# Performance work log

Hardware: AMD Instinct MI355X
Metric: run time of the kernel (lower is better)

## Reference

```python
import jax, jax.numpy as jnp
import numpy as np

ITERS = 4
LN_EPS = 1e-5


def build_grid(H, W):
    # standard uORF grid in [-1, 1], shape (H, W, 2), last dim = (x, y)
    x = jnp.linspace(-1.0 + 1.0 / W, 1.0 - 1.0 / W, W)
    y = jnp.linspace(-1.0 + 1.0 / H, 1.0 - 1.0 / H, H)
    yy, xx = jnp.meshgrid(y, x, indexing='ij')
    return jnp.stack([xx, yy], axis=-1)


def ln(x, g, b):
    m = jnp.mean(x, axis=-1, keepdims=True)
    v = jnp.var(x, axis=-1, keepdims=True)
    return (x - m) * jax.lax.rsqrt(v + LN_EPS) * g + b


def setup_inputs():
    key = jax.random.key(0)
    ks = jax.random.split(key, 16)
    B, H, W, C, K, Ds = 4, 64, 64, 256, 5, 256
    s = 0.02
    inp = {
        'feat': jax.random.normal(ks[0], (B, H, W, C), jnp.float32),
        'mask': (jax.random.uniform(ks[1], (K, 1, H, W)) > 0.5).astype(jnp.float32),
        'noise': jax.random.normal(ks[2], (B, K, Ds), jnp.float32),
        'slots_mu': jax.random.normal(ks[3], (1, 1, Ds), jnp.float32),
        'slots_logsigma': jax.random.normal(ks[4], (1, 1, Ds), jnp.float32) * s,
        'norm_g': jnp.ones((C,), jnp.float32), 'norm_b': jnp.zeros((C,), jnp.float32),
        'grid_W': jax.random.normal(ks[5], (C, 4), jnp.float32) * s,
        'grid_b': jnp.zeros((C,), jnp.float32),
        'k_W': jax.random.normal(ks[6], (C, C), jnp.float32) * s,
        'v_W': jax.random.normal(ks[7], (C, C), jnp.float32) * s,
        'mlp_g': jnp.ones((C,), jnp.float32), 'mlp_b': jnp.zeros((C,), jnp.float32),
        'mlp_W': jax.random.normal(ks[8], (Ds, C), jnp.float32) * s,
        'mlp_bias': jnp.zeros((Ds,), jnp.float32),
        'q_g': jnp.ones((Ds,), jnp.float32), 'q_b': jnp.zeros((Ds,), jnp.float32),
        'q_W': jax.random.normal(ks[9], (Ds, Ds), jnp.float32) * s,
        'gru_Wih': jax.random.normal(ks[10], (3 * Ds, Ds), jnp.float32) * s,
        'gru_Whh': jax.random.normal(ks[11], (3 * Ds, Ds), jnp.float32) * s,
        'gru_bih': jnp.zeros((3 * Ds,), jnp.float32),
        'gru_bhh': jnp.zeros((3 * Ds,), jnp.float32),
        'res_g': jnp.ones((Ds,), jnp.float32), 'res_b': jnp.zeros((Ds,), jnp.float32),
        'res_W': jax.random.normal(ks[12], (Ds, Ds), jnp.float32) * s,
        'res_bias': jnp.zeros((Ds,), jnp.float32),
    }
    return inp


def reference(feat, mask, noise, slots_mu, slots_logsigma, norm_g, norm_b,
              grid_W, grid_b, k_W, v_W, mlp_g, mlp_b, mlp_W, mlp_bias,
              q_g, q_b, q_W, gru_Wih, gru_Whh, gru_bih, gru_bhh,
              res_g, res_b, res_W, res_bias):
    B, H, W, C = feat.shape
    K = mask.shape[0]
    N = H * W
    Ds = slots_mu.shape[-1]
    scale = Ds ** -0.5

    grid = build_grid(H, W)                                   # (H, W, 2)
    # foreground positions: mask-weighted mean of grid -> (K, 2)
    g = jnp.transpose(grid, (2, 0, 1))[None]                  # (1, 2, H, W)
    fg_pos = jnp.sum(g * mask, axis=(2, 3)) / (jnp.sum(mask, axis=(2, 3)) + 1e-5)
    fg_pos = jnp.broadcast_to(fg_pos[None], (B, K, 2))        # (B, K, 2)

    feat_n = ln(feat.reshape(B, N, C), norm_g, norm_b)        # (B, N, C)
    mask_flat = mask.reshape(K, N)
    slot = slots_mu + jnp.exp(slots_logsigma) * noise         # (B, K, Ds)

    # k, v with relative position embedding; fg_pos never changes in-loop,
    # so compute once (the original recomputes the same values each iter).
    rel = grid.reshape(1, 1, N, 2) - fg_pos[:, :, None, :]    # (B, K, N, 2)
    rel4 = jnp.concatenate([rel, -rel], axis=-1)              # (B, K, N, 4)
    ge = rel4 @ grid_W.T + grid_b                             # (B, K, N, C)
    kbase = feat_n @ k_W.T                                    # (B, N, C)
    vbase = feat_n @ v_W.T
    kk = ln(kbase[:, None] + ge, mlp_g, mlp_b) @ mlp_W.T + mlp_bias  # (B,K,N,Ds)
    vv = ln(vbase[:, None] + ge, mlp_g, mlp_b) @ mlp_W.T + mlp_bias

    attn_vis = None
    for _ in range(ITERS):
        slot_prev = slot
        q = ln(slot, q_g, q_b) @ q_W.T                        # (B, K, Ds)
        attn = jnp.einsum('bkd,bknd->bkn', q, kk) * scale
        attn = jnp.where(mask_flat[None] == 0, -1e9, attn)
        attn = jax.nn.softmax(attn, axis=-1)                  # (B, K, N)
        upd = jnp.einsum('bkn,bknd->bkd', attn, vv)           # (B, K, Ds)
        # torch GRUCell
        x = upd.reshape(-1, Ds)
        h = slot.reshape(-1, Ds)
        gi = x @ gru_Wih.T + gru_bih
        gh = h @ gru_Whh.T + gru_bhh
        ir, iz, inn = jnp.split(gi, 3, axis=-1)
        hr, hz, hn = jnp.split(gh, 3, axis=-1)
        r = jax.nn.sigmoid(ir + hr)
        z = jax.nn.sigmoid(iz + hz)
        n = jnp.tanh(inn + r * hn)
        hnew = ((1.0 - z) * n + z * h).reshape(B, K, Ds)
        slot = (ln(hnew, res_g, res_b) @ res_W.T + res_bias) + slot_prev
        amin = attn.min(axis=-1, keepdims=True)
        amax = attn.max(axis=-1, keepdims=True)
        attn_vis = (attn - amin) / (amax - amin + 1e-5)
    return slot, fg_pos, attn_vis
```

## Files before the change

### kernel.cpp

```cpp
#include <hip/hip_runtime.h>
#include <math.h>

typedef unsigned short u16;
typedef unsigned int   u32;
typedef short bf8v __attribute__((ext_vector_type(8)));
typedef float f4v  __attribute__((ext_vector_type(4)));

static constexpr int B_=4, C_=256, K_=5, D_=256, N_=4096, IT_=4;
static constexpr int LP_=264;
static constexpr int PREP_N=2839;
static constexpr float EPS_=1e-5f;

__device__ __forceinline__ float bf2f(u16 u){ u32 x=((u32)u)<<16; float f; __builtin_memcpy(&f,&x,4); return f; }
__device__ __forceinline__ float bflo(u32 u){ u32 x=u<<16; float f; __builtin_memcpy(&f,&x,4); return f; }
__device__ __forceinline__ float bfhi(u32 u){ u32 x=u&0xffff0000u; float f; __builtin_memcpy(&f,&x,4); return f; }
__device__ __forceinline__ u16 f2bf(float f){ u32 x; __builtin_memcpy(&x,&f,4); u32 r=x+0x7fffu+((x>>16)&1u); return (u16)(r>>16); }
__device__ __forceinline__ float ldin(const void* p, size_t i, int f){
  return f ? ((const float*)p)[i] : bf2f(((const u16*)p)[i]);
}
__device__ __forceinline__ void stout(void* p, size_t i, float v, int f){
  if (f) ((float*)p)[i]=v; else ((u16*)p)[i]=f2bf(v);
}

__device__ __forceinline__ void breduce4(float&a,float&b,float&c,float&d,float* red){
  #pragma unroll
  for(int o=32;o>0;o>>=1){
    a+=__shfl_down(a,o,64); b+=__shfl_down(b,o,64);
    c+=__shfl_down(c,o,64); d+=__shfl_down(d,o,64);
  }
  int w=threadIdx.x>>6;
  __syncthreads();
  if((threadIdx.x&63)==0){ red[w]=a; red[4+w]=b; red[8+w]=c; red[12+w]=d; }
  __syncthreads();
  a=red[0]+red[1]+red[2]+red[3];
  b=red[4]+red[5]+red[6]+red[7];
  c=red[8]+red[9]+red[10]+red[11];
  d=red[12]+red[13]+red[14]+red[15];
}
__device__ __forceinline__ void breduce4_16(float&a,float&b,float&c,float&d,float* red){
  #pragma unroll
  for(int o=32;o>0;o>>=1){
    a+=__shfl_down(a,o,64); b+=__shfl_down(b,o,64);
    c+=__shfl_down(c,o,64); d+=__shfl_down(d,o,64);
  }
  int w=threadIdx.x>>6;
  __syncthreads();
  if((threadIdx.x&63)==0){ red[w]=a; red[16+w]=b; red[32+w]=c; red[48+w]=d; }
  __syncthreads();
  a=0;b=0;c=0;d=0;
  #pragma unroll
  for(int i=0;i<16;++i){ a+=red[i]; b+=red[16+i]; c+=red[32+i]; d+=red[48+i]; }
}

__device__ __forceinline__ int probe_f(const void* feat, float* red){
  const u32* p=(const u32*)feat;
  int t=threadIdx.x; int bad=0;
  #pragma unroll
  for(int s=0;s<8;++s){
    u32 wd=p[t+s*256];
    float lo=bf2f((u16)(wd&0xffffu));
    if(!(fabsf(lo)<1e6f)) bad++;
  }
  float bb=(float)bad, z1=0,z2=0,z3=0;
  breduce4(bb,z1,z2,z3,red);
  return (bb>=16.f)?1:0;
}

__global__ void prep1_kernel(const void* feat,
    const void* kW, const void* vW, const void* mW, const void* qW, const void* rW,
    const void* Wih, const void* Whh, const void* mu, const void* lsig, const void* noise,
    const void* gW, const void* gb_, const void* mg,
    const void* mb_, const void* mbias, const void* mask,
    int* flag, float* WqT, float* WrT, float* WihT, float* WhhT,
    float* slot, float* gvec,
    u16* Wkb, u16* Wvb, u16* Wgb,
    float* Uvec, float* Qs, float* fg, void* out)
{
  __shared__ float redp[16];
  int bid=blockIdx.x;
  int t=threadIdx.x;
  int f=probe_f(feat, redp);
  if(bid==0 && t==0) *flag=f;
  __syncthreads();
  if(bid<PREP_N){
    int e=bid*256+t;
    if(e<65536){ int c=e>>8, r=e&255; WqT[e]=ldin(qW,(size_t)r*256+c,f); return;} e-=65536;
    if(e<65536){ int c=e>>8, r=e&255; WrT[e]=ldin(rW,(size_t)r*256+c,f); return;} e-=65536;
    if(e<196608){ int c=e/768, r=e-c*768; WihT[e]=ldin(Wih,(size_t)r*256+c,f); return;} e-=196608;
    if(e<196608){ int c=e/768, r=e-c*768; WhhT[e]=ldin(Whh,(size_t)r*256+c,f); return;} e-=196608;
    if(e<5120){ int d=e&255; slot[e]=ldin(mu,d,f)+expf(ldin(lsig,d,f))*ldin(noise,e,f); return;} e-=5120;
    if(e<768){
      int c=e&255, sel=e>>8;
      float v;
      if(sel==0)      v=ldin(gW,c*4+0,f)-ldin(gW,c*4+2,f);
      else if(sel==1) v=ldin(gW,c*4+1,f)-ldin(gW,c*4+3,f);
      else            v=ldin(gb_,c,f);
      gvec[e]=v; return;
    } e-=768;
    if(e<65536){ Wkb[e]=f2bf(ldin(kW,e,f)); return;} e-=65536;
    if(e<65536){ Wvb[e]=f2bf(ldin(vW,e,f)); return;} e-=65536;
    if(e<65536){ int c=e&255; Wgb[e]=f2bf(ldin(mg,c,f)*ldin(mW,e,f)); }
    return;
  }
  __shared__ float s_a[256], s_b[256], s_c[256];
  if(bid==PREP_N){
    s_a[t]=ldin(gW,t*4+0,f)-ldin(gW,t*4+2,f);
    s_b[t]=ldin(gW,t*4+1,f)-ldin(gW,t*4+3,f);
    s_c[t]=ldin(gb_,t,f);
    __syncthreads();
    float u1=0,u2=0,u3=0,gw=0,bw=0;
    #pragma unroll 8
    for(int c=0;c<256;++c){
      float mwv=ldin(mW,(size_t)t*256+c,f);
      float wg=ldin(mg,c,f)*mwv;
      u1+=s_a[c]*wg; u2+=s_b[c]*wg; u3+=s_c[c]*wg; gw+=wg;
      bw+=ldin(mb_,c,f)*mwv;
    }
    Uvec[t]=u1; Uvec[256+t]=u2; Uvec[512+t]=u3; Uvec[768+t]=gw;
    Uvec[1024+t]=bw+ldin(mbias,t,f);
    float a=s_a[t], b=s_b[t], cc=s_c[t];
    float s0=a*a,s1=b*b,s2=cc*cc,s3=a*b; breduce4(s0,s1,s2,s3,redp);
    float s4=a*cc,s5=b*cc,s6=a,s7=b;     breduce4(s4,s5,s6,s7,redp);
    float s8=cc,z1=0,z2=0,z3=0;          breduce4(s8,z1,z2,z3,redp);
    if(t==0){
      Qs[0]=s0; Qs[1]=s1; Qs[2]=s2; Qs[3]=s3; Qs[4]=s4; Qs[5]=s5;
      Qs[6]=s6*(1.f/256.f); Qs[7]=s7*(1.f/256.f); Qs[8]=s8*(1.f/256.f);
    }
  } else {
    int k=bid-PREP_N-1;
    float sx=0,sy=0,sm=0;
    for(int s=0;s<16;++s){
      int p=t+s*256;
      float m=ldin(mask,(size_t)k*N_+p,f);
      int i=p>>6, j=p&63;
      float x=(2*j+1)*(1.0f/64.0f)-1.0f;
      float y=(2*i+1)*(1.0f/64.0f)-1.0f;
      sx+=x*m; sy+=y*m; sm+=m;
    }
    float d=0;
    breduce4(sx,sy,sm,d,redp);
    if(t==0){
      float inv=1.0f/(sm+1e-5f);
      float fx=sx*inv, fy=sy*inv;
      fg[k*2]=fx; fg[k*2+1]=fy;
      for(int b=0;b<B_;++b){
        stout(out, 5120+(b*K_+k)*2+0, fx, f);
        stout(out, 5120+(b*K_+k)*2+1, fy, f);
      }
    }
  }
}

__global__ void __launch_bounds__(256) base_kernel(const int* flag, const void* feat, const void* ng, const void* nb,
    const u16* Wkb, const u16* Wvb, const u16* Wgb, const float* gvec,
    float* scal, u16* PkT, u16* Pvb,
    const float* slot, const void* qg, const void* qb_, const float* WqT,
    float* qbuf)
{
  __shared__ u16 fnb[16*LP_];
  __shared__ u16 kbL[16*LP_];
  __shared__ u16 vbL[16*LP_];
  int t=threadIdx.x, f=*flag;
  if(blockIdx.x>=1024){
    float* Lq=(float*)fnb; float* red=(float*)vbL;
    int bk=blockIdx.x-1024;
    float x=slot[bk*256+t];
    float s=x,s2=x*x,z0=0,z1=0; breduce4(s,s2,z0,z1,red);
    float m=s*(1.f/256.f), v=s2*(1.f/256.f)-m*m;
    Lq[t]=(x-m)*rsqrtf(v+EPS_)*ldin(qg,t,f)+ldin(qb_,t,f);
    __syncthreads();
    float acc=0;
    #pragma unroll 8
    for(int c=0;c<256;++c) acc+=Lq[c]*WqT[c*256+t];
    qbuf[bk*256+t]=acc;
    return;
  }
  int w=t>>6, l=t&63;
  int quad=l>>4, m=l&15;
  int row0=blockIdx.x*16;
  {
    float g0=ldin(ng,l,f), g1=ldin(ng,l+64,f), g2=ldin(ng,l+128,f), g3=ldin(ng,l+192,f);
    float b0=ldin(nb,l,f), b1=ldin(nb,l+64,f), b2=ldin(nb,l+128,f), b3=ldin(nb,l+192,f);
    #pragma unroll
    for(int r4=0;r4<4;++r4){
      int r=4*w+r4; size_t base=(size_t)(row0+r)*256;
      float x0=ldin(feat,base+l,f), x1=ldin(feat,base+l+64,f),
            x2=ldin(feat,base+l+128,f), x3=ldin(feat,base+l+192,f);
      float s=x0+x1+x2+x3, s2=x0*x0+x1*x1+x2*x2+x3*x3;
      #pragma unroll
      for(int o=32;o>0;o>>=1){ s+=__shfl_xor(s,o,64); s2+=__shfl_xor(s2,o,64); }
      float mm=s*(1.f/256.f), inv=rsqrtf(s2*(1.f/256.f)-mm*mm+EPS_);
      fnb[r*LP_+l]    =f2bf((x0-mm)*inv*g0+b0);
      fnb[r*LP_+l+64] =f2bf((x1-mm)*inv*g1+b1);
      fnb[r*LP_+l+128]=f2bf((x2-mm)*inv*g2+b2);
      fnb[r*LP_+l+192]=f2bf((x3-mm)*inv*g3+b3);
    }
  }
  __syncthreads();
  {
    f4v ack[4], acv[4];
    #pragma unroll
    for(int i=0;i<4;++i){ ack[i]=(f4v){0.f,0.f,0.f,0.f}; acv[i]=(f4v){0.f,0.f,0.f,0.f}; }
    #pragma unroll
    for(int kk=0;kk<8;++kk){
      int kb0=kk*32+quad*8;
      bf8v af=*(bf8v*)&fnb[m*LP_+kb0];
      #pragma unroll
      for(int i=0;i<4;++i){
        int n=64*w+16*i+m;
        bf8v bk=*(const bf8v*)(Wkb+(size_t)n*256+kb0);
        bf8v bv=*(const bf8v*)(Wvb+(size_t)n*256+kb0);
        ack[i]=__builtin_amdgcn_mfma_f32_16x16x32_bf16(af,bk,ack[i],0,0,0);
        acv[i]=__builtin_amdgcn_mfma_f32_16x16x32_bf16(af,bv,acv[i],0,0,0);
      }
    }
    #pragma unroll
    for(int i=0;i<4;++i){
      int n=64*w+16*i+m;
      #pragma unroll
      for(int r=0;r<4;++r){
        int row=quad*4+r;
        kbL[row*LP_+n]=f2bf(ack[i][r]);
        vbL[row*LP_+n]=f2bf(acv[i][r]);
      }
    }
  }
  __syncthreads();
  {
    float gA0=gvec[l], gA1=gvec[l+64], gA2=gvec[l+128], gA3=gvec[l+192];
    float gB0=gvec[256+l], gB1=gvec[256+l+64], gB2=gvec[256+l+128], gB3=gvec[256+l+192];
    float gC0=gvec[512+l], gC1=gvec[512+l+64], gC2=gvec[512+l+128], gC3=gvec[512+l+192];
    for(int r4=0;r4<4;++r4){
      int r=4*w+r4;
      float k0=bf2f(kbL[r*LP_+l]), k1=bf2f(kbL[r*LP_+l+64]),
            k2=bf2f(kbL[r*LP_+l+128]), k3=bf2f(kbL[r*LP_+l+192]);
      float x0=bf2f(vbL[r*LP_+l]), x1=bf2f(vbL[r*LP_+l+64]),
            x2=bf2f(vbL[r*LP_+l+128]), x3=bf2f(vbL[r*LP_+l+192]);
      float v0=k0+k1+k2+k3;
      float v1=k0*k0+k1*k1+k2*k2+k3*k3;
      float v2=k0*gA0+k1*gA1+k2*gA2+k3*gA3;
      float v3=k0*gB0+k1*gB1+k2*gB2+k3*gB3;
      float v4=k0*gC0+k1*gC1+k2*gC2+k3*gC3;
      float v5=x0+x1+x2+x3;
      float v6=x0*x0+x1*x1+x2*x2+x3*x3;
      float v7=x0*gA0+x1*gA1+x2*gA2+x3*gA3;
      float v8=x0*gB0+x1*gB1+x2*gB2+x3*gB3;
      float v9=x0*gC0+x1*gC1+x2*gC2+x3*gC3;
      #pragma unroll
      for(int o=32;o>0;o>>=1){
        v0+=__shfl_down(v0,o,64); v1+=__shfl_down(v1,o,64); v2+=__shfl_down(v2,o,64);
        v3+=__shfl_down(v3,o,64); v4+=__shfl_down(v4,o,64); v5+=__shfl_down(v5,o,64);
        v6+=__shfl_down(v6,o,64); v7+=__shfl_down(v7,o,64); v8+=__shfl_down(v8,o,64);
        v9+=__shfl_down(v9,o,64);
      }
      if(l==0){
        float* sc=scal+(size_t)(row0+r)*10;
        sc[0]=v0; sc[1]=v1; sc[2]=v2; sc[3]=v3; sc[4]=v4;
        sc[5]=v5; sc[6]=v6; sc[7]=v7; sc[8]=v8; sc[9]=v9;
      }
    }
  }
  {
    f4v apk[4], apv[4];
    #pragma unroll
    for(int i=0;i<4;++i){ apk[i]=(f4v){0.f,0.f,0.f,0.f}; apv[i]=(f4v){0.f,0.f,0.f,0.f}; }
    #pragma unroll
    for(int kk=0;kk<8;++kk){
      int kb0=kk*32+quad*8;
      bf8v afk=*(bf8v*)&kbL[m*LP_+kb0];
      bf8v afv=*(bf8v*)&vbL[m*LP_+kb0];
      #pragma unroll
      for(int i=0;i<4;++i){
        int n=64*w+16*i+m;
        bf8v bg=*(const bf8v*)(Wgb+(size_t)n*256+kb0);
        apk[i]=__builtin_amdgcn_mfma_f32_16x16x32_bf16(afk,bg,apk[i],0,0,0);
        apv[i]=__builtin_amdgcn_mfma_f32_16x16x32_bf16(afv,bg,apv[i],0,0,0);
      }
    }
    #pragma unroll
    for(int i=0;i<4;++i){
      int d=64*w+16*i+m;
      *(ushort4*)(PkT+(size_t)d*16384+row0+quad*4)=
        make_ushort4(f2bf(apk[i][0]),f2bf(apk[i][1]),f2bf(apk[i][2]),f2bf(apk[i][3]));
      #pragma unroll
      for(int r=0;r<4;++r)
        fnb[(quad*4+r)*LP_+d]=f2bf(apv[i][r]);
    }
  }
  __syncthreads();
  {
    int d0=l*4;
    #pragma unroll
    for(int r=0;r<4;++r){
      int row=4*w+r;
      ushort4 s4=make_ushort4(fnb[row*LP_+d0],fnb[row*LP_+d0+1],fnb[row*LP_+d0+2],fnb[row*LP_+d0+3]);
      *(ushort4*)(Pvb+(size_t)(row0+row)*256+d0)=s4;
    }
  }
}

__global__ void __launch_bounds__(512) attn_kernel(const int* flag, const float* qbuf, const u16* PkT,
    const float* scal, const float* Qs, const float* Uvec, const float* fg, const void* mask,
    const u16* Pvb, float* logits, float* pmax, float* psum, float* updpart, float* sscp,
    int store_lg)
{
  __shared__ float q5[1280];
  __shared__ float un[10240];
  __shared__ float lgs[320], ivs[320], mvs[320];
  __shared__ float qs5[40], fgs[10], Qss[9], MSl[5];
  __shared__ float sred[8][5][4];
  int tid=threadIdx.x, f=*flag;
  int b=blockIdx.x>>6, ch=blockIdx.x&63;
  int w=tid>>6, l=tid&63;
  int n0=ch<<6;
  for(int p=tid;p<1280;p+=512) q5[p]=qbuf[(size_t)b*1280+p];
  if(tid<10) fgs[tid]=fg[tid];
  if(tid<9)  Qss[tid]=Qs[tid];
  __syncthreads();
  for(int p=w;p<25;p+=8){
    int k=p/5, j=p%5;
    float s=q5[k*256+l]*Uvec[j*256+l]+q5[k*256+l+64]*Uvec[j*256+l+64]
           +q5[k*256+l+128]*Uvec[j*256+l+128]+q5[k*256+l+192]*Uvec[j*256+l+192];
    #pragma unroll
    for(int o=32;o>0;o>>=1) s+=__shfl_xor(s,o,64);
    if(l==0) qs5[k*8+j]=s;
  }
  {
    int n=n0+l; size_t row=(size_t)b*N_+n;
    float dk0=0,dk1=0,dk2=0,dk3=0,dk4=0;
    int cbase=w*32;
    #pragma unroll 8
    for(int cc=0;cc<32;++cc){
      int c=cbase+cc;
      float pv=bf2f(PkT[(size_t)c*16384+row]);
      dk0+=pv*q5[c]; dk1+=pv*q5[256+c]; dk2+=pv*q5[512+c];
      dk3+=pv*q5[768+c]; dk4+=pv*q5[1024+c];
    }
    un[(w*5+0)*64+l]=dk0; un[(w*5+1)*64+l]=dk1; un[(w*5+2)*64+l]=dk2;
    un[(w*5+3)*64+l]=dk3; un[(w*5+4)*64+l]=dk4;
  }
  __syncthreads();
  if(tid<320){
    int k=tid>>6, nl=tid&63;
    float dot=0;
    #pragma unroll
    for(int j=0;j<8;++j) dot+=un[(j*5+k)*64+nl];
    int n2=n0+nl; size_t row2=(size_t)b*N_+n2;
    const float* sc=scal+row2*10;
    float rx=(2*(n2&63)+1)*(1.f/64.f)-1.f-fgs[2*k];
    float ry=(2*(n2>>6)+1)*(1.f/64.f)-1.f-fgs[2*k+1];
    float qge=rx*rx*Qss[0]+ry*ry*Qss[1]+Qss[2]+2.f*(rx*ry*Qss[3]+rx*Qss[4]+ry*Qss[5]);
    float mk=sc[0]*(1.f/256.f)+rx*Qss[6]+ry*Qss[7]+Qss[8];
    float sxk=sc[1]+2.f*(rx*sc[2]+ry*sc[3]+sc[4])+qge;
    float invK=rsqrtf(sxk*(1.f/256.f)-mk*mk+EPS_);
    float lg=invK*(dot+rx*qs5[k*8+0]+ry*qs5[k*8+1]+qs5[k*8+2]-mk*qs5[k*8+3])+qs5[k*8+4];
    float mval=ldin(mask,(size_t)k*N_+n2,f);
    lg=(mval==0.f)? -1e9f : lg*0.0625f;
    if(store_lg) logits[((size_t)(b*5+k))*N_+n2]=lg;
    lgs[tid]=lg;
    float mv=sc[5]*(1.f/256.f)+rx*Qss[6]+ry*Qss[7]+Qss[8];
    float sxv=sc[6]+2.f*(rx*sc[7]+ry*sc[8]+sc[9])+qge;
    mvs[tid]=mv;
    ivs[tid]=rsqrtf(sxv*(1.f/256.f)-mv*mv+EPS_);
  }
  __syncthreads();
  if(tid<64){
    #pragma unroll
    for(int k=0;k<5;++k){
      float v=lgs[k*64+tid];
      float M=v;
      #pragma unroll
      for(int o=32;o>0;o>>=1) M=fmaxf(M,__shfl_xor(M,o,64));
      float e=expf(v-M);
      #pragma unroll
      for(int o=32;o>0;o>>=1) e+=__shfl_xor(e,o,64);
      if(tid==0){ pmax[((size_t)(b*64+ch))*5+k]=M; psum[((size_t)(b*64+ch))*5+k]=e; MSl[k]=M; }
    }
  }
  __syncthreads();
  {
    float acc[5][4]={{0}};
    float swx[5]={0,0,0,0,0}, swy[5]={0,0,0,0,0}, sw[5]={0,0,0,0,0}, swm[5]={0,0,0,0,0};
    #pragma unroll 2
    for(int rr=0;rr<8;++rr){
      int nl=w*8+rr; int n2=n0+nl;
      size_t row=(size_t)b*N_+n2;
      uint2 pu=*(const uint2*)(Pvb+row*256+l*4);
      float px=bflo(pu.x), py=bfhi(pu.x), pz=bflo(pu.y), pw=bfhi(pu.y);
      int jx=n2&63, iy=n2>>6;
      #pragma unroll
      for(int k=0;k<5;++k){
        float wgt=expf(lgs[k*64+nl]-MSl[k])*ivs[k*64+nl];
        float rx=(2*jx+1)*(1.f/64.f)-1.f-fgs[2*k];
        float ry=(2*iy+1)*(1.f/64.f)-1.f-fgs[2*k+1];
        acc[k][0]+=wgt*px; acc[k][1]+=wgt*py; acc[k][2]+=wgt*pz; acc[k][3]+=wgt*pw;
        sw[k]+=wgt; swx[k]+=wgt*rx; swy[k]+=wgt*ry; swm[k]+=wgt*mvs[k*64+nl];
      }
    }
    #pragma unroll
    for(int k=0;k<5;++k)
      *(float4*)&un[(w*5+k)*256+l*4]=make_float4(acc[k][0],acc[k][1],acc[k][2],acc[k][3]);
    if(l==0){
      #pragma unroll
      for(int k=0;k<5;++k){ sred[w][k][0]=swx[k]; sred[w][k][1]=swy[k];
                            sred[w][k][2]=sw[k];  sred[w][k][3]=swm[k]; }
    }
  }
  __syncthreads();
  for(int p=tid;p<1280;p+=512){
    int k=p>>8, d=p&255;
    float v=0;
    #pragma unroll
    for(int j=0;j<8;++j) v+=un[(j*5+k)*256+d];
    updpart[((size_t)blockIdx.x*5+k)*256+d]=v;
  }
  if(tid<20){
    int kk=tid>>2, j=tid&3;
    float s=0;
    #pragma unroll
    for(int jj=0;jj<8;++jj) s+=sred[jj][kk][j];
    sscp[((size_t)blockIdx.x*5+kk)*4+j]=s;
  }
}

__global__ void __launch_bounds__(1024) gru_kernel(const int* flag, float* slot, const float* updpart,
    const float* sscp, const float* Uvec, const float* pmax, const float* psum, const float* logits,
    const float* WihT, const float* WhhT, const void* bih, const void* bhh,
    const void* rg, const void* rb_, const float* WrT, const void* rbias,
    const void* qg, const void* qb_, const float* WqT, float* qbuf,
    int do_vis, void* out)
{
  __shared__ float u[256], h[256], sn[256];
  __shared__ float part[4][6][256];
  __shared__ float red[64];
  __shared__ float cvec[4];
  __shared__ float fch[64];
  __shared__ float MSg[2];
  int tid=threadIdx.x, t=tid&255, g=tid>>8;
  int blk=blockIdx.x;
  int f=*flag;
  if(blk>=20){
    if(!do_vis) return;
    int bk2=blk-20, k2=bk2%K_, b2=bk2/K_;
    if(tid<64){
      float pm=pmax[((size_t)(b2*64+tid))*5+k2];
      float ps=psum[((size_t)(b2*64+tid))*5+k2];
      float M=pm;
      #pragma unroll
      for(int o=32;o>0;o>>=1) M=fmaxf(M,__shfl_xor(M,o,64));
      float e=ps*expf(pm-M);
      #pragma unroll
      for(int o=32;o>0;o>>=1) e+=__shfl_xor(e,o,64);
      if(tid==0){ MSg[0]=M; MSg[1]=1.0f/e; }
    }
    __syncthreads();
    float M=MSg[0], Sinv=MSg[1];
    float a[4]; float mn=1e30f, mx=-1e30f;
    #pragma unroll
    for(int s=0;s<4;++s){
      a[s]=expf(logits[(size_t)bk2*N_+tid+s*1024]-M)*Sinv;
      mn=fminf(mn,a[s]); mx=fmaxf(mx,a[s]);
    }
    #pragma unroll
    for(int o=32;o>0;o>>=1){ mn=fminf(mn,__shfl_down(mn,o,64)); mx=fmaxf(mx,__shfl_down(mx,o,64)); }
    int wv=tid>>6;
    __syncthreads();
    if((tid&63)==0){ red[wv]=mn; red[16+wv]=mx; }
    __syncthreads();
    mn=1e30f; mx=-1e30f;
    #pragma unroll
    for(int i=0;i<16;++i){ mn=fminf(mn,red[i]); mx=fmaxf(mx,red[16+i]); }
    float inv=1.0f/(mx-mn+1e-5f);
    #pragma unroll
    for(int s=0;s<4;++s) stout(out, 5160+(size_t)bk2*N_+tid+s*1024, (a[s]-mn)*inv, f);
    return;
  }
  int bk=blk, k=bk%K_, b=bk/K_;
  if(tid<64){
    float pm=pmax[((size_t)(b*64+tid))*5+k];
    float ps=psum[((size_t)(b*64+tid))*5+k];
    float M=pm;
    #pragma unroll
    for(int o=32;o>0;o>>=1) M=fmaxf(M,__shfl_xor(M,o,64));
    float fc=expf(pm-M);
    fch[tid]=fc;
    float e=ps*fc;
    #pragma unroll
    for(int o=32;o>0;o>>=1) e+=__shfl_xor(e,o,64);
    if(tid==0){ MSg[0]=M; MSg[1]=1.0f/e; }
  }
  __syncthreads();
  float Sinv=MSg[1];
  float ua=0;
  {
    int ch0=g*16;
    #pragma unroll 4
    for(int ci=0;ci<16;++ci){ int ch=ch0+ci; ua += fch[ch]*updpart[(((size_t)(b*64+ch))*5+k)*256+t]; }
  }
  part[g][0][t]=ua;
  if(t<4){
    float s=0;
    #pragma unroll 4
    for(int ci=0;ci<16;++ci){ int ch=g*16+ci; s += fch[ch]*sscp[(((size_t)(b*64+ch))*5+k)*4+t]; }
    part[g][1][t]=s;
  }
  __syncthreads();
  if(g==0 && t<4) cvec[t]=part[0][1][t]+part[1][1][t]+part[2][1][t]+part[3][1][t];
  __syncthreads();
  if(g==0){
    float uu=part[0][0][t]+part[1][0][t]+part[2][0][t]+part[3][0][t];
    u[t]=(uu+cvec[0]*Uvec[t]+cvec[1]*Uvec[256+t]+cvec[2]*Uvec[512+t]-cvec[3]*Uvec[768+t])*Sinv
         +Uvec[1024+t];
    h[t]=slot[bk*256+t];
  }
  __syncthreads();
  float p0=0,p1=0,p2=0,p3=0,p4=0,p5=0;
  int c0=g*64;
  #pragma unroll 8
  for(int cc=0;cc<64;++cc){
    int c=c0+cc;
    float uc=u[c], hc=h[c];
    const float* wi=WihT+(size_t)c*768+t;
    const float* wh=WhhT+(size_t)c*768+t;
    p0+=uc*wi[0]; p1+=uc*wi[256]; p2+=uc*wi[512];
    p3+=hc*wh[0]; p4+=hc*wh[256]; p5+=hc*wh[512];
  }
  part[g][0][t]=p0; part[g][1][t]=p1; part[g][2][t]=p2;
  part[g][3][t]=p3; part[g][4][t]=p4; part[g][5][t]=p5;
  __syncthreads();
  float hn=0;
  if(g==0){
    float gi0=ldin(bih,t,f)+part[0][0][t]+part[1][0][t]+part[2][0][t]+part[3][0][t];
    float gi1=ldin(bih,256+t,f)+part[0][1][t]+part[1][1][t]+part[2][1][t]+part[3][1][t];
    float gi2=ldin(bih,512+t,f)+part[0][2][t]+part[1][2][t]+part[2][2][t]+part[3][2][t];
    float gh0=ldin(bhh,t,f)+part[0][3][t]+part[1][3][t]+part[2][3][t]+part[3][3][t];
    float gh1=ldin(bhh,256+t,f)+part[0][4][t]+part[1][4][t]+part[2][4][t]+part[3][4][t];
    float gh2=ldin(bhh,512+t,f)+part[0][5][t]+part[1][5][t]+part[2][5][t]+part[3][5][t];
    float r=1.f/(1.f+expf(-(gi0+gh0)));
    float z=1.f/(1.f+expf(-(gi1+gh1)));
    float nn=tanhf(gi2+r*gh2);
    hn=(1.f-z)*nn+z*h[t];
  }
  float s=hn, sq=hn*hn, za=0, zb=0;
  breduce4_16(s,sq,za,zb,red);
  if(g==0){
    float m=s*(1.f/256.f), var=sq*(1.f/256.f)-m*m;
    u[t]=(hn-m)*rsqrtf(var+EPS_)*ldin(rg,t,f)+ldin(rb_,t,f);
  }
  __syncthreads();
  float pr=0;
  #pragma unroll 8
  for(int cc=0;cc<64;++cc){ int c=c0+cc; pr+=u[c]*WrT[(size_t)c*256+t]; }
  part[g][0][t]=pr;
  __syncthreads();
  if(g==0){
    float acc=ldin(rbias,t,f)+h[t]+part[0][0][t]+part[1][0][t]+part[2][0][t]+part[3][0][t];
    slot[bk*256+t]=acc;
    stout(out, (size_t)bk*256+t, acc, f);
    sn[t]=acc;
  }
  __syncthreads();
  float xs=(g==0)? sn[t]:0.f;
  float xq=xs*xs, zc=0, zd=0;
  breduce4_16(xs,xq,zc,zd,red);
  if(g==0){
    float m=xs*(1.f/256.f), var=xq*(1.f/256.f)-m*m;
    u[t]=(sn[t]-m)*rsqrtf(var+EPS_)*ldin(qg,t,f)+ldin(qb_,t,f);
  }
  __syncthreads();
  float pq=0;
  #pragma unroll 8
  for(int cc=0;cc<64;++cc){ int c=c0+cc; pq+=u[c]*WqT[(size_t)c*256+t]; }
  part[g][0][t]=pq;
  __syncthreads();
  if(g==0){
    float qv=part[0][0][t]+part[1][0][t]+part[2][0][t]+part[3][0][t];
    qbuf[bk*256+t]=qv;
  }
}

extern "C" void kernel_launch(void* const* d_in, const int* in_sizes, int n_in,
                              void* d_out, int out_size, void* d_ws, size_t ws_size,
                              hipStream_t stream)
{
  const void* feat =d_in[0];  const void* mask =d_in[1];  const void* noise=d_in[2];
  const void* mu   =d_in[3];  const void* lsig =d_in[4];  const void* ng   =d_in[5];
  const void* nb   =d_in[6];  const void* gW   =d_in[7];  const void* gb_  =d_in[8];
  const void* kW   =d_in[9];  const void* vW   =d_in[10]; const void* mg   =d_in[11];
  const void* mb_  =d_in[12]; const void* mW   =d_in[13]; const void* mbias=d_in[14];
  const void* qg   =d_in[15]; const void* qb_  =d_in[16]; const void* qW   =d_in[17];
  const void* Wih  =d_in[18]; const void* Whh  =d_in[19]; const void* bih  =d_in[20];
  const void* bhh  =d_in[21]; const void* rg   =d_in[22]; const void* rb_  =d_in[23];
  const void* rW   =d_in[24]; const void* rbias=d_in[25];

  char* p=(char*)d_ws;
  auto alloc=[&](size_t bytes)->char*{ char* r=p; p+=(bytes+255)&~(size_t)255; return r; };
  int*   flag   =(int*)  alloc(256);
  float* fg     =(float*)alloc(64);
  float* slot   =(float*)alloc(5120*4);
  float* qbuf   =(float*)alloc(5120*4);
  float* logits =(float*)alloc((size_t)81920*4);
  float* pmax   =(float*)alloc(1280*4);
  float* psum   =(float*)alloc(1280*4);
  float* updpart=(float*)alloc((size_t)256*5*256*4);
  float* sscp   =(float*)alloc((size_t)256*5*4*4);
  float* WqT    =(float*)alloc((size_t)65536*4);
  float* WrT    =(float*)alloc((size_t)65536*4);
  float* WihT   =(float*)alloc((size_t)196608*4);
  float* WhhT   =(float*)alloc((size_t)196608*4);
  float* gvec   =(float*)alloc(768*4);
  float* Uvec   =(float*)alloc(1280*4);
  float* Qs     =(float*)alloc(64);
  float* scal   =(float*)alloc((size_t)163840*4);
  u16*   Wkb    =(u16*)  alloc((size_t)65536*2);
  u16*   Wvb    =(u16*)  alloc((size_t)65536*2);
  u16*   Wgb    =(u16*)  alloc((size_t)65536*2);
  u16*   PkT    =(u16*)  alloc((size_t)16384*256*2);
  u16*   Pvb    =(u16*)  alloc((size_t)16384*256*2);

  prep1_kernel<<<PREP_N+6,256,0,stream>>>(feat,kW,vW,mW,qW,rW,Wih,Whh,mu,lsig,noise,gW,gb_,mg,
                                          mb_,mbias,mask,
                                          flag,WqT,WrT,WihT,WhhT,slot,gvec,Wkb,Wvb,Wgb,
                                          Uvec,Qs,fg,d_out);
  base_kernel<<<1044,256,0,stream>>>(flag,feat,ng,nb,Wkb,Wvb,Wgb,gvec,scal,PkT,Pvb,
                                     slot,qg,qb_,WqT,qbuf);
  for(int it=0; it<IT_; ++it){
    attn_kernel<<<B_*64,512,0,stream>>>(flag,qbuf,PkT,scal,Qs,Uvec,fg,mask,Pvb,
                                        logits,pmax,psum,updpart,sscp,(it==IT_-1)?1:0);
    int nb_g = (it==IT_-1)? 40 : 20;
    gru_kernel<<<nb_g,1024,0,stream>>>(flag,slot,updpart,sscp,Uvec,pmax,psum,logits,
                                       WihT,WhhT,bih,bhh,rg,rb_,WrT,rbias,
                                       qg,qb_,WqT,qbuf,(it==IT_-1)?1:0,d_out);
  }
}
```

Measured before the change: 385.7 us.

## Retile base kernel to 64-row blocks with swizzled LDS and register-reused MFMA fragments

Each base_kernel block now processes 64 rows with 512 threads instead of 16 rows with 256 threads. Every weight fragment loaded from global memory feeds four row tiles, so weight traffic per row drops roughly fourfold. The padded LDS arrays become two 32 KB dynamic buffers with an XOR swizzle, and the feature loads are vectorised. The block count falls from 1044 to 276, which may leave the GPU underoccupied, and the larger dynamic LDS per block limits residency.

New measurement: 372.7 us. 3.4% less time.

```diff
diff --git a/kernel.cpp b/kernel.cpp
--- a/kernel.cpp
+++ b/kernel.cpp
@@ -7,7 +7,6 @@
 typedef float f4v  __attribute__((ext_vector_type(4)));
 
 static constexpr int B_=4, C_=256, K_=5, D_=256, N_=4096, IT_=4;
-static constexpr int LP_=264;
 static constexpr int PREP_N=2839;
 static constexpr float EPS_=1e-5f;
 
@@ -20,6 +19,9 @@
 }
 __device__ __forceinline__ void stout(void* p, size_t i, float v, int f){
   if (f) ((float*)p)[i]=v; else ((u16*)p)[i]=f2bf(v);
+}
+__device__ __forceinline__ int sw16(int row,int col){
+  return row*256 + ((((col>>3)^(row&7))<<3) | (col&7));
 }
 
 __device__ __forceinline__ void breduce4(float&a,float&b,float&c,float&d,float* red){
@@ -151,91 +153,125 @@
   }
 }
 
-__global__ void __launch_bounds__(256) base_kernel(const int* flag, const void* feat, const void* ng, const void* nb,
+__global__ void __launch_bounds__(512,2) base_kernel(const int* flag, const void* feat, const void* ng, const void* nb,
     const u16* Wkb, const u16* Wvb, const u16* Wgb, const float* gvec,
     float* scal, u16* PkT, u16* Pvb,
     const float* slot, const void* qg, const void* qb_, const float* WqT,
     float* qbuf)
 {
-  __shared__ u16 fnb[16*LP_];
-  __shared__ u16 kbL[16*LP_];
-  __shared__ u16 vbL[16*LP_];
+  extern __shared__ u16 smem[];
+  u16* bufA = smem;
+  u16* bufB = smem + 16384;
   int t=threadIdx.x, f=*flag;
-  if(blockIdx.x>=1024){
-    float* Lq=(float*)fnb; float* red=(float*)vbL;
-    int bk=blockIdx.x-1024;
-    float x=slot[bk*256+t];
-    float s=x,s2=x*x,z0=0,z1=0; breduce4(s,s2,z0,z1,red);
-    float m=s*(1.f/256.f), v=s2*(1.f/256.f)-m*m;
-    Lq[t]=(x-m)*rsqrtf(v+EPS_)*ldin(qg,t,f)+ldin(qb_,t,f);
-    __syncthreads();
-    float acc=0;
+  if(blockIdx.x>=256){
+    float* Lq =(float*)smem;
+    float* pp =(float*)smem+256;
+    float* red=(float*)smem+768;
+    int bk=blockIdx.x-256;
+    int tt=t&255, hh=t>>8, w=t>>6;
+    float x=slot[bk*256+tt];
+    float s=x, s2=x*x;
+    #pragma unroll
+    for(int o=32;o>0;o>>=1){ s+=__shfl_down(s,o,64); s2+=__shfl_down(s2,o,64); }
+    if((t&63)==0){ red[w]=s; red[8+w]=s2; }
+    __syncthreads();
+    s=0; s2=0;
+    #pragma unroll
+    for(int i=0;i<8;++i){ s+=red[i]; s2+=red[8+i]; }
+    float m=s*(1.f/512.f), v=s2*(1.f/512.f)-m*m;
+    float lq=(x-m)*rsqrtf(v+EPS_)*ldin(qg,tt,f)+ldin(qb_,tt,f);
+    if(hh==0) Lq[tt]=lq;
+    __syncthreads();
+    float acc=0; int cb=hh*128;
     #pragma unroll 8
-    for(int c=0;c<256;++c) acc+=Lq[c]*WqT[c*256+t];
-    qbuf[bk*256+t]=acc;
+    for(int cc=0;cc<128;++cc){ int c=cb+cc; acc+=Lq[c]*WqT[(size_t)c*256+tt]; }
+    pp[hh*256+tt]=acc;
+    __syncthreads();
+    if(hh==0) qbuf[bk*256+tt]=pp[tt]+pp[256+tt];
     return;
   }
   int w=t>>6, l=t&63;
   int quad=l>>4, m=l&15;
-  int row0=blockIdx.x*16;
+  int row0=blockIdx.x*64;
   {
-    float g0=ldin(ng,l,f), g1=ldin(ng,l+64,f), g2=ldin(ng,l+128,f), g3=ldin(ng,l+192,f);
-    float b0=ldin(nb,l,f), b1=ldin(nb,l+64,f), b2=ldin(nb,l+128,f), b3=ldin(nb,l+192,f);
-    #pragma unroll
-    for(int r4=0;r4<4;++r4){
-      int r=4*w+r4; size_t base=(size_t)(row0+r)*256;
-      float x0=ldin(feat,base+l,f), x1=ldin(feat,base+l+64,f),
-            x2=ldin(feat,base+l+128,f), x3=ldin(feat,base+l+192,f);
+    float g0=ldin(ng,4*l+0,f), g1=ldin(ng,4*l+1,f), g2=ldin(ng,4*l+2,f), g3=ldin(ng,4*l+3,f);
+    float b0=ldin(nb,4*l+0,f), b1=ldin(nb,4*l+1,f), b2=ldin(nb,4*l+2,f), b3=ldin(nb,4*l+3,f);
+    #pragma unroll
+    for(int r8=0;r8<8;++r8){
+      int row=8*w+r8;
+      float x0,x1,x2,x3;
+      if(f){
+        float4 v4=((const float4*)feat)[(size_t)(row0+row)*64+l];
+        x0=v4.x; x1=v4.y; x2=v4.z; x3=v4.w;
+      } else {
+        ushort4 uu=((const ushort4*)feat)[(size_t)(row0+row)*64+l];
+        x0=bf2f(uu.x); x1=bf2f(uu.y); x2=bf2f(uu.z); x3=bf2f(uu.w);
+      }
       float s=x0+x1+x2+x3, s2=x0*x0+x1*x1+x2*x2+x3*x3;
       #pragma unroll
       for(int o=32;o>0;o>>=1){ s+=__shfl_xor(s,o,64); s2+=__shfl_xor(s2,o,64); }
       float mm=s*(1.f/256.f), inv=rsqrtf(s2*(1.f/256.f)-mm*mm+EPS_);
-      fnb[r*LP_+l]    =f2bf((x0-mm)*inv*g0+b0);
-      fnb[r*LP_+l+64] =f2bf((x1-mm)*inv*g1+b1);
-      fnb[r*LP_+l+128]=f2bf((x2-mm)*inv*g2+b2);
-      fnb[r*LP_+l+192]=f2bf((x3-mm)*inv*g3+b3);
+      ushort4 o4=make_ushort4(f2bf((x0-mm)*inv*g0+b0), f2bf((x1-mm)*inv*g1+b1),
+                              f2bf((x2-mm)*inv*g2+b2), f2bf((x3-mm)*inv*g3+b3));
+      *(ushort4*)&bufA[sw16(row,4*l)]=o4;
     }
   }
   __syncthreads();
   {
-    f4v ack[4], acv[4];
-    #pragma unroll
-    for(int i=0;i<4;++i){ ack[i]=(f4v){0.f,0.f,0.f,0.f}; acv[i]=(f4v){0.f,0.f,0.f,0.f}; }
+    f4v ack[4][2], acv[4][2];
+    #pragma unroll
+    for(int rt=0;rt<4;++rt)
+      #pragma unroll
+      for(int i=0;i<2;++i){ ack[rt][i]=(f4v){0.f,0.f,0.f,0.f}; acv[rt][i]=(f4v){0.f,0.f,0.f,0.f}; }
     #pragma unroll
     for(int kk=0;kk<8;++kk){
-      int kb0=kk*32+quad*8;
-      bf8v af=*(bf8v*)&fnb[m*LP_+kb0];
-      #pragma unroll
-      for(int i=0;i<4;++i){
-        int n=64*w+16*i+m;
-        bf8v bk=*(const bf8v*)(Wkb+(size_t)n*256+kb0);
-        bf8v bv=*(const bf8v*)(Wvb+(size_t)n*256+kb0);
-        ack[i]=__builtin_amdgcn_mfma_f32_16x16x32_bf16(af,bk,ack[i],0,0,0);
-        acv[i]=__builtin_amdgcn_mfma_f32_16x16x32_bf16(af,bv,acv[i],0,0,0);
-      }
-    }
-    #pragma unroll
-    for(int i=0;i<4;++i){
-      int n=64*w+16*i+m;
-      #pragma unroll
-      for(int r=0;r<4;++r){
-        int row=quad*4+r;
-        kbL[row*LP_+n]=f2bf(ack[i][r]);
-        vbL[row*LP_+n]=f2bf(acv[i][r]);
-      }
-    }
+      int kcol=kk*32+quad*8;
+      bf8v af[4];
+      #pragma unroll
+      for(int rt=0;rt<4;++rt) af[rt]=*(bf8v*)&bufA[sw16(rt*16+m,kcol)];
+      #pragma unroll
+      for(int i=0;i<2;++i){
+        int n=w*32+16*i+m;
+        bf8v bk=*(const bf8v*)(Wkb+(size_t)n*256+kcol);
+        bf8v bv=*(const bf8v*)(Wvb+(size_t)n*256+kcol);
+        #pragma unroll
+        for(int rt=0;rt<4;++rt){
+          ack[rt][i]=__builtin_amdgcn_mfma_f32_16x16x32_bf16(af[rt],bk,ack[rt][i],0,0,0);
+          acv[rt][i]=__builtin_amdgcn_mfma_f32_16x16x32_bf16(af[rt],bv,acv[rt][i],0,0,0);
+        }
+      }
+    }
+    #pragma unroll
+    for(int rt=0;rt<4;++rt)
+      #pragma unroll
+      for(int i=0;i<2;++i){
+        int n=w*32+16*i+m;
+        #pragma unroll
+        for(int r=0;r<4;++r)
+          bufB[sw16(rt*16+quad*4+r,n)]=f2bf(ack[rt][i][r]);
+      }
+    __syncthreads();
+    #pragma unroll
+    for(int rt=0;rt<4;++rt)
+      #pragma unroll
+      for(int i=0;i<2;++i){
+        int n=w*32+16*i+m;
+        #pragma unroll
+        for(int r=0;r<4;++r)
+          bufA[sw16(rt*16+quad*4+r,n)]=f2bf(acv[rt][i][r]);
+      }
   }
   __syncthreads();
   {
     float gA0=gvec[l], gA1=gvec[l+64], gA2=gvec[l+128], gA3=gvec[l+192];
     float gB0=gvec[256+l], gB1=gvec[256+l+64], gB2=gvec[256+l+128], gB3=gvec[256+l+192];
     float gC0=gvec[512+l], gC1=gvec[512+l+64], gC2=gvec[512+l+128], gC3=gvec[512+l+192];
-    for(int r4=0;r4<4;++r4){
-      int r=4*w+r4;
-      float k0=bf2f(kbL[r*LP_+l]), k1=bf2f(kbL[r*LP_+l+64]),
-            k2=bf2f(kbL[r*LP_+l+128]), k3=bf2f(kbL[r*LP_+l+192]);
-      float x0=bf2f(vbL[r*LP_+l]), x1=bf2f(vbL[r*LP_+l+64]),
-            x2=bf2f(vbL[r*LP_+l+128]), x3=bf2f(vbL[r*LP_+l+192]);
+    for(int r8=0;r8<8;++r8){
+      int row=8*w+r8;
+      float k0=bf2f(bufB[sw16(row,l)]),     k1=bf2f(bufB[sw16(row,l+64)]),
+            k2=bf2f(bufB[sw16(row,l+128)]), k3=bf2f(bufB[sw16(row,l+192)]);
+      float x0=bf2f(bufA[sw16(row,l)]),     x1=bf2f(bufA[sw16(row,l+64)]),
+            x2=bf2f(bufA[sw16(row,l+128)]), x3=bf2f(bufA[sw16(row,l+192)]);
       float v0=k0+k1+k2+k3;
       float v1=k0*k0+k1*k1+k2*k2+k3*k3;
       float v2=k0*gA0+k1*gA1+k2*gA2+k3*gA3;
@@ -254,48 +290,63 @@
         v9+=__shfl_down(v9,o,64);
       }
       if(l==0){
-        float* sc=scal+(size_t)(row0+r)*10;
+        float* sc=scal+(size_t)(row0+row)*10;
         sc[0]=v0; sc[1]=v1; sc[2]=v2; sc[3]=v3; sc[4]=v4;
         sc[5]=v5; sc[6]=v6; sc[7]=v7; sc[8]=v8; sc[9]=v9;
       }
     }
   }
   {
-    f4v apk[4], apv[4];
-    #pragma unroll
-    for(int i=0;i<4;++i){ apk[i]=(f4v){0.f,0.f,0.f,0.f}; apv[i]=(f4v){0.f,0.f,0.f,0.f}; }
+    f4v apk[4][2], apv[4][2];
+    #pragma unroll
+    for(int rt=0;rt<4;++rt)
+      #pragma unroll
+      for(int i=0;i<2;++i){ apk[rt][i]=(f4v){0.f,0.f,0.f,0.f}; apv[rt][i]=(f4v){0.f,0.f,0.f,0.f}; }
     #pragma unroll
     for(int kk=0;kk<8;++kk){
-      int kb0=kk*32+quad*8;
-      bf8v afk=*(bf8v*)&kbL[m*LP_+kb0];
-      bf8v afv=*(bf8v*)&vbL[m*LP_+kb0];
-      #pragma unroll
-      for(int i=0;i<4;++i){
-        int n=64*w+16*i+m;
-        bf8v bg=*(const bf8v*)(Wgb+(size_t)n*256+kb0);
-        apk[i]=__builtin_amdgcn_mfma_f32_16x16x32_bf16(afk,bg,apk[i],0,0,0);
-        apv[i]=__builtin_amdgcn_mfma_f32_16x16x32_bf16(afv,bg,apv[i],0,0,0);
-      }
-    }
-    #pragma unroll
-    for(int i=0;i<4;++i){
-      int d=64*w+16*i+m;
-      *(ushort4*)(PkT+(size_t)d*16384+row0+quad*4)=
-        make_ushort4(f2bf(apk[i][0]),f2bf(apk[i][1]),f2bf(apk[i][2]),f2bf(apk[i][3]));
-      #pragma unroll
-      for(int r=0;r<4;++r)
-        fnb[(quad*4+r)*LP_+d]=f2bf(apv[i][r]);
-    }
-  }
-  __syncthreads();
-  {
-    int d0=l*4;
-    #pragma unroll
-    for(int r=0;r<4;++r){
-      int row=4*w+r;
-      ushort4 s4=make_ushort4(fnb[row*LP_+d0],fnb[row*LP_+d0+1],fnb[row*LP_+d0+2],fnb[row*LP_+d0+3]);
-      *(ushort4*)(Pvb+(size_t)(row0+row)*256+d0)=s4;
-    }
+      int kcol=kk*32+quad*8;
+      bf8v afk[4], afv[4];
+      #pragma unroll
+      for(int rt=0;rt<4;++rt){
+        afk[rt]=*(bf8v*)&bufB[sw16(rt*16+m,kcol)];
+        afv[rt]=*(bf8v*)&bufA[sw16(rt*16+m,kcol)];
+      }
+      #pragma unroll
+      for(int i=0;i<2;++i){
+        int n=w*32+16*i+m;
+        bf8v bg=*(const bf8v*)(Wgb+(size_t)n*256+kcol);
+        #pragma unroll
+        for(int rt=0;rt<4;++rt){
+          apk[rt][i]=__builtin_amdgcn_mfma_f32_16x16x32_bf16(afk[rt],bg,apk[rt][i],0,0,0);
+          apv[rt][i]=__builtin_amdgcn_mfma_f32_16x16x32_bf16(afv[rt],bg,apv[rt][i],0,0,0);
+        }
+      }
+    }
+    #pragma unroll
+    for(int rt=0;rt<4;++rt)
+      #pragma unroll
+      for(int i=0;i<2;++i){
+        int d=w*32+16*i+m;
+        *(ushort4*)(PkT+(size_t)d*16384+row0+rt*16+quad*4)=
+          make_ushort4(f2bf(apk[rt][i][0]),f2bf(apk[rt][i][1]),f2bf(apk[rt][i][2]),f2bf(apk[rt][i][3]));
+      }
+    __syncthreads();
+    #pragma unroll
+    for(int rt=0;rt<4;++rt)
+      #pragma unroll
+      for(int i=0;i<2;++i){
+        int d=w*32+16*i+m;
+        #pragma unroll
+        for(int r=0;r<4;++r)
+          bufB[sw16(rt*16+quad*4+r,d)]=f2bf(apv[rt][i][r]);
+      }
+  }
+  __syncthreads();
+  #pragma unroll
+  for(int r8=0;r8<8;++r8){
+    int row=8*w+r8;
+    ushort4 s4=*(ushort4*)&bufB[sw16(row,4*l)];
+    *(ushort4*)(Pvb+(size_t)(row0+row)*256+4*l)=s4;
   }
 }
 
@@ -622,8 +673,8 @@
                                           mb_,mbias,mask,
                                           flag,WqT,WrT,WihT,WhhT,slot,gvec,Wkb,Wvb,Wgb,
                                           Uvec,Qs,fg,d_out);
-  base_kernel<<<1044,256,0,stream>>>(flag,feat,ng,nb,Wkb,Wvb,Wgb,gvec,scal,PkT,Pvb,
-                                     slot,qg,qb_,WqT,qbuf);
+  base_kernel<<<276,512,65536,stream>>>(flag,feat,ng,nb,Wkb,Wvb,Wgb,gvec,scal,PkT,Pvb,
+                                        slot,qg,qb_,WqT,qbuf);
   for(int it=0; it<IT_; ++it){
     attn_kernel<<<B_*64,512,0,stream>>>(flag,qbuf,PkT,scal,Qs,Uvec,fg,mask,Pvb,
                                         logits,pmax,psum,updpart,sscp,(it==IT_-1)?1:0);
```
